# Kernel tuning notes

Hardware: AMD Instinct MI355X
Metric: run time of the kernel (lower is better)

## Reference

```python
import jax, jax.numpy as jnp
import numpy as np

D_MODEL = 1024
NUM_HEADS = 16
D_K = D_MODEL // NUM_HEADS
B, S = 4, 2048
NEG = -1e20


def setup_inputs() -> dict:
    key = jax.random.key(0)
    ks = jax.random.split(key, 12)
    def lin(kw, kb):
        # torch nn.Linear init: U(-1/sqrt(in), 1/sqrt(in)), weight shape [out, in]
        bound = 1.0 / np.sqrt(D_MODEL)
        W = jax.random.uniform(kw, (D_MODEL, D_MODEL), jnp.float32, -bound, bound)
        b = jax.random.uniform(kb, (D_MODEL,), jnp.float32, -bound, bound)
        return W, b
    Wq, bq = lin(ks[0], ks[1])
    Wk, bk = lin(ks[2], ks[3])
    Wv, bv = lin(ks[4], ks[5])
    Wo, bo = lin(ks[6], ks[7])
    q = jax.random.normal(ks[8], (B, S, D_MODEL), jnp.float32)
    k = jax.random.normal(ks[9], (B, S, D_MODEL), jnp.float32)
    v = jax.random.normal(ks[10], (B, S, D_MODEL), jnp.float32)
    # causal mask, broadcastable [1,1,S,S]; mask==0 positions are masked out
    mask = jnp.tril(jnp.ones((S, S), jnp.int32))[None, None]
    return {"q": q, "k": k, "v": v, "mask": mask,
            "Wq": Wq, "bq": bq, "Wk": Wk, "bk": bk,
            "Wv": Wv, "bv": bv, "Wo": Wo, "bo": bo}


def _split_heads(x):
    b, s, _ = x.shape
    return x.reshape(b, s, NUM_HEADS, D_K).transpose(0, 2, 1, 3)  # [b,h,s,dk]


def reference(q, k, v, mask, Wq, bq, Wk, bk, Wv, bv, Wo, bo):
    qh = _split_heads(q @ Wq.T + bq)
    kh = _split_heads(k @ Wk.T + bk)
    vh = _split_heads(v @ Wv.T + bv)
    scores = jnp.einsum('bhqd,bhkd->bhqk', qh, kh) / jnp.sqrt(jnp.float32(D_K))
    scores = jnp.where(mask == 0, jnp.float32(NEG), scores)
    attn = jax.nn.softmax(scores, axis=-1)  # dropout is identity in eval mode
    out = jnp.einsum('bhqk,bhkd->bhqd', attn, vh)
    out = out.transpose(0, 2, 1, 3).reshape(q.shape[0], -1, D_MODEL)
    return out @ Wo.T + bo, attn
```

## Files before the change

### kernel.cpp

```cpp
#include <hip/hip_runtime.h>
#include <stdint.h>

#define S_LEN 2048
#define NHEADS 16
#define DK 64
#define DMODEL 1024
#define PS_STRIDE 72
#define S_MASK -3.0e4f

typedef __bf16 bf16;
typedef __bf16 bf16x8 __attribute__((ext_vector_type(8)));
typedef float f32x4 __attribute__((ext_vector_type(4)));
typedef uint32_t u32;

#define MFMA(a, b, c) __builtin_amdgcn_mfma_f32_16x16x32_bf16((a), (b), (c), 0, 0, 0)

#define WAVE_LGKM0()                                       \
  do {                                                     \
    asm volatile("s_waitcnt lgkmcnt(0)" ::: "memory");     \
    __builtin_amdgcn_sched_barrier(0);                     \
  } while (0)
#define BAR_VM16()                                         \
  do {                                                     \
    asm volatile("s_waitcnt vmcnt(16)" ::: "memory");      \
    __builtin_amdgcn_sched_barrier(0);                     \
    __builtin_amdgcn_s_barrier();                          \
    __builtin_amdgcn_sched_barrier(0);                     \
  } while (0)

__device__ __forceinline__ bf16x8 cvt8(f32x4 a, f32x4 b) {
  bf16x8 w;
  w[0] = (bf16)a[0]; w[1] = (bf16)a[1]; w[2] = (bf16)a[2]; w[3] = (bf16)a[3];
  w[4] = (bf16)b[0]; w[5] = (bf16)b[1]; w[6] = (bf16)b[2]; w[7] = (bf16)b[3];
  return w;
}

__device__ __forceinline__ void async16(const void* g, void* lds_uniform) {
  __builtin_amdgcn_global_load_lds((const __attribute__((address_space(1))) u32*)g,
                                   (__attribute__((address_space(3))) u32*)lds_uniform,
                                   16, 0, 0);
}

__device__ __forceinline__ void stage_tile8(const bf16* gbase, size_t rstride,
                                            bf16* buf, int wave, int lane) {
  int c = wave * 64 + lane;
  int r = c >> 3, ch = c & 7;
  int chg = ch ^ (r & 7);
  const bf16* src = gbase + (size_t)r * rstride + chg * 8;
  char* dst = (char*)buf + (size_t)(wave * 64) * 16;
  async16(src, dst);
}

__global__ __launch_bounds__(256) void cvt_f32_bf16(const float* __restrict__ src,
                                                    bf16* __restrict__ dst, int n8) {
  int stride = gridDim.x * blockDim.x;
  for (int i = blockIdx.x * blockDim.x + threadIdx.x; i < n8; i += stride) {
    f32x4 a = ((const f32x4*)src)[2 * i];
    f32x4 b = ((const f32x4*)src)[2 * i + 1];
    ((bf16x8*)dst)[i] = cvt8(a, b);
  }
}

template <int MODE, typename OutT>
__global__ __launch_bounds__(256, 2) void gemm_bias(const bf16* __restrict__ X,
                                                    const bf16* __restrict__ W,
                                                    const float* __restrict__ bias,
                                                    OutT* __restrict__ out) {
  __shared__ __attribute__((aligned(16))) bf16 At[128 * 32];
  __shared__ __attribute__((aligned(16))) bf16 Bt[128 * 32];
  const int tid = threadIdx.x;
  const int wave = tid >> 6;
  const int lane = tid & 63;
  const int col16 = lane & 15;
  const int kg = lane >> 4;
  const int m0 = blockIdx.x * 128;
  const int n0 = blockIdx.y * 128;
  const int wm = (wave >> 1) * 64;
  const int wn = (wave & 1) * 64;

  f32x4 acc[4][4] = {};

  for (int k0 = 0; k0 < 1024; k0 += 32) {
    __syncthreads();
#pragma unroll
    for (int is = 0; is < 2; ++is) {
      int idx = wave * 64 + is * 256 + lane;
      int row = idx >> 2, ch = idx & 3;
      const char* ga = (const char*)(X + (size_t)(m0 + row) * 1024 + k0) + ch * 16;
      const char* gb = (const char*)(W + (size_t)(n0 + row) * 1024 + k0) + ch * 16;
      async16(ga, (char*)At + (size_t)(wave * 64 + is * 256) * 16);
      async16(gb, (char*)Bt + (size_t)(wave * 64 + is * 256) * 16);
    }
    __syncthreads();

    bf16x8 af[4], bfr[4];
#pragma unroll
    for (int i = 0; i < 4; ++i)
      af[i] = *(const bf16x8*)&At[(wm + i * 16 + col16) * 32 + kg * 8];
#pragma unroll
    for (int j = 0; j < 4; ++j)
      bfr[j] = *(const bf16x8*)&Bt[(wn + j * 16 + col16) * 32 + kg * 8];
#pragma unroll
    for (int i = 0; i < 4; ++i)
#pragma unroll
      for (int j = 0; j < 4; ++j) acc[i][j] = MFMA(af[i], bfr[j], acc[i][j]);
  }

#pragma unroll
  for (int j = 0; j < 4; ++j) {
    int n = n0 + wn + j * 16 + col16;
    float bj = bias[n];
#pragma unroll
    for (int i = 0; i < 4; ++i) {
#pragma unroll
      for (int r = 0; r < 4; ++r) {
        int m = m0 + wm + i * 16 + kg * 4 + r;
        float v = acc[i][j][r] + bj;
        size_t o;
        if (MODE == 0) {
          o = (size_t)m * 1024 + n;
        } else {
          int b = m >> 11, s = m & 2047;
          int h = n >> 6, d = n & 63;
          if (MODE == 1)
            o = ((size_t)(b * 16 + h) * 2048 + s) * 64 + d;
          else
            o = ((size_t)(b * 16 + h) * 64 + d) * 2048 + s;
        }
        out[o] = (OutT)v;
      }
    }
  }
}

__global__ __launch_bounds__(512, 4) void attn_fused(const bf16* __restrict__ Qh,
                                                     const bf16* __restrict__ Kh,
                                                     const bf16* __restrict__ Vt,
                                                     float* __restrict__ attn,
                                                     bf16* __restrict__ O) {
  __shared__ __attribute__((aligned(16))) bf16 Klds[2][64 * 64];
  __shared__ __attribute__((aligned(16))) bf16 Vlds[2][64 * 64];
  __shared__ __attribute__((aligned(16))) bf16 Ps[128 * PS_STRIDE];
  const int tid = threadIdx.x;
  const int wave = tid >> 6;
  const int lane = tid & 63;
  const int col16 = lane & 15;
  const int kg = lane >> 4;
  const int pr = blockIdx.x;
  const int bh = blockIdx.z * NHEADS + blockIdx.y;

  const bf16* qb = Qh + (size_t)bh * S_LEN * DK;
  const bf16* kb = Kh + (size_t)bh * S_LEN * DK;
  const bf16* vb = Vt + (size_t)bh * DK * S_LEN;
  float* ab = attn + (size_t)bh * S_LEN * S_LEN;
  const int b_ = bh >> 4, h_ = bh & 15;

#pragma unroll 1
  for (int sp = 0; sp < 2; ++sp) {
    const int bq = sp ? (15 - pr) : pr;
    const int q0 = bq * 128;
    const int jt_max = 2 * bq + 1;

    bf16x8 qf[2];
#pragma unroll
    for (int kk = 0; kk < 2; ++kk) {
      bf16x8 v = *(const bf16x8*)&qb[(size_t)(q0 + wave * 16 + col16) * DK + kk * 32 + kg * 8];
      bf16x8 sc;
#pragma unroll
      for (int e = 0; e < 8; ++e) sc[e] = (bf16)((float)v[e] * 0.125f);
      qf[kk] = sc;
    }

    float l_run[4] = {};

    for (int jt = 0; jt <= jt_max; ++jt) {
      const int j0 = jt * 64;
      f32x4 s[4] = {};
#pragma unroll
      for (int kk = 0; kk < 2; ++kk) {
        bf16x8 kf[4];
#pragma unroll
        for (int fc = 0; fc < 4; ++fc)
          kf[fc] = *(const bf16x8*)&kb[(size_t)(j0 + fc * 16 + col16) * DK + kk * 32 + kg * 8];
#pragma unroll
        for (int fc = 0; fc < 4; ++fc) s[fc] = MFMA(qf[kk], kf[fc], s[fc]);
      }
      if (jt >= 2 * bq) {
#pragma unroll
        for (int fc = 0; fc < 4; ++fc)
#pragma unroll
          for (int r = 0; r < 4; ++r) {
            int qi = q0 + wave * 16 + kg * 4 + r;
            int j = j0 + fc * 16 + col16;
            if (j > qi) s[fc][r] = S_MASK;
          }
      }
#pragma unroll
      for (int r = 0; r < 4; ++r)
        l_run[r] += (__expf(s[0][r]) + __expf(s[1][r])) + (__expf(s[2][r]) + __expf(s[3][r]));
    }
    float linv[4];
#pragma unroll
    for (int r = 0; r < 4; ++r) {
      float l = l_run[r];
#pragma unroll
      for (int dd = 1; dd < 16; dd <<= 1) l += __shfl_xor(l, dd, 64);
      linv[r] = 1.f / l;
    }

    {
      f32x4 z = {0.f, 0.f, 0.f, 0.f};
      for (int jt = jt_max + 1; jt < S_LEN / 64; ++jt) {
        const int j0 = jt * 64;
#pragma unroll
        for (int rep = 0; rep < 4; ++rep) {
          int idx = rep * 512 + tid;
          int row = idx >> 4, c = idx & 15;
          *(f32x4*)&ab[(size_t)(q0 + row) * S_LEN + j0 + c * 4] = z;
        }
      }
    }

    f32x4 o[4] = {};
    stage_tile8(kb, DK, Klds[0], wave, lane);
    stage_tile8(vb, S_LEN, Vlds[0], wave, lane);
    __syncthreads();
    int cur = 0;
    for (int jt = 0; jt <= jt_max; ++jt) {
      if (jt < jt_max) {
        stage_tile8(kb + (size_t)(jt + 1) * 64 * DK, DK, Klds[cur ^ 1], wave, lane);
        stage_tile8(vb + (jt + 1) * 64, S_LEN, Vlds[cur ^ 1], wave, lane);
      }
      const int j0 = jt * 64;
      f32x4 s[4] = {};
#pragma unroll
      for (int kk = 0; kk < 2; ++kk) {
        bf16x8 kf[4];
#pragma unroll
        for (int fc = 0; fc < 4; ++fc) {
          int rr = fc * 16 + col16;
          kf[fc] = *(const bf16x8*)&Klds[cur][rr * 64 + (((kk << 2) + kg) ^ (rr & 7)) * 8];
        }
#pragma unroll
        for (int fc = 0; fc < 4; ++fc) s[fc] = MFMA(qf[kk], kf[fc], s[fc]);
      }
      if (jt >= 2 * bq) {
#pragma unroll
        for (int fc = 0; fc < 4; ++fc)
#pragma unroll
          for (int r = 0; r < 4; ++r) {
            int qi = q0 + wave * 16 + kg * 4 + r;
            int j = j0 + fc * 16 + col16;
            if (j > qi) s[fc][r] = S_MASK;
          }
      }
#pragma unroll
      for (int fc = 0; fc < 4; ++fc)
#pragma unroll
        for (int r = 0; r < 4; ++r) {
          float p = __expf(s[fc][r]) * linv[r];
          int row = wave * 16 + kg * 4 + r;
          int col = fc * 16 + col16;
          ab[(size_t)(q0 + row) * S_LEN + j0 + col] = p;
          Ps[row * PS_STRIDE + col] = (bf16)p;
        }
      WAVE_LGKM0();
#pragma unroll
      for (int kk = 0; kk < 2; ++kk) {
        bf16x8 pf, vf[4];
        pf = *(const bf16x8*)&Ps[(wave * 16 + col16) * PS_STRIDE + kk * 32 + kg * 8];
#pragma unroll
        for (int fc = 0; fc < 4; ++fc) {
          int rr = fc * 16 + col16;
          vf[fc] = *(const bf16x8*)&Vlds[cur][rr * 64 + (((kk << 2) + kg) ^ (rr & 7)) * 8];
        }
#pragma unroll
        for (int fc = 0; fc < 4; ++fc) o[fc] = MFMA(pf, vf[fc], o[fc]);
      }
      BAR_VM16();
      cur ^= 1;
    }

#pragma unroll
    for (int fc = 0; fc < 4; ++fc)
#pragma unroll
      for (int r = 0; r < 4; ++r) {
        size_t row = (size_t)b_ * S_LEN + q0 + wave * 16 + kg * 4 + r;
        O[row * DMODEL + h_ * 64 + fc * 16 + col16] = (bf16)o[fc][r];
      }
    __syncthreads();
  }
}

static inline void cvt_launch(const float* src, bf16* dst, size_t n, hipStream_t stream) {
  int n8 = (int)(n / 8);
  int blocks = (n8 + 255) / 256;
  if (blocks > 2048) blocks = 2048;
  cvt_f32_bf16<<<blocks, 256, 0, stream>>>(src, dst, n8);
}

extern "C" void kernel_launch(void* const* d_in, const int* in_sizes, int n_in,
                              void* d_out, int out_size, void* d_ws, size_t ws_size,
                              hipStream_t stream) {
  (void)in_sizes; (void)n_in; (void)out_size; (void)ws_size;
  const float* q = (const float*)d_in[0];
  const float* k = (const float*)d_in[1];
  const float* v = (const float*)d_in[2];
  const float* Wq = (const float*)d_in[4];
  const float* bq = (const float*)d_in[5];
  const float* Wk = (const float*)d_in[6];
  const float* bk = (const float*)d_in[7];
  const float* Wv = (const float*)d_in[8];
  const float* bv = (const float*)d_in[9];
  const float* Wo = (const float*)d_in[10];
  const float* bo = (const float*)d_in[11];

  float* out = (float*)d_out;
  float* attn = out + (size_t)8192 * 1024;

  const size_t NX = (size_t)8192 * 1024;
  const size_t NW = (size_t)1024 * 1024;
  bf16* Qh = (bf16*)d_ws;
  bf16* Kh = Qh + NX;
  bf16* Vt = Kh + NX;
  bf16* O = Vt + NX;
  bf16* Xbf = O + NX;
  bf16* Wbf = Xbf + NX;

  dim3 gg(64, 8), bb(256);

  cvt_launch(q, Xbf, NX, stream);
  cvt_launch(Wq, Wbf, NW, stream);
  gemm_bias<1, bf16><<<gg, bb, 0, stream>>>(Xbf, Wbf, bq, Qh);

  cvt_launch(k, Xbf, NX, stream);
  cvt_launch(Wk, Wbf, NW, stream);
  gemm_bias<1, bf16><<<gg, bb, 0, stream>>>(Xbf, Wbf, bk, Kh);

  cvt_launch(v, Xbf, NX, stream);
  cvt_launch(Wv, Wbf, NW, stream);
  gemm_bias<2, bf16><<<gg, bb, 0, stream>>>(Xbf, Wbf, bv, Vt);

  attn_fused<<<dim3(8, NHEADS, 4), 512, 0, stream>>>(Qh, Kh, Vt, attn, O);

  cvt_launch(Wo, Wbf, NW, stream);
  gemm_bias<0, float><<<gg, bb, 0, stream>>>(O, Wbf, bo, out);
}
```

Baseline: 529.4 us.

## Process paired high/low query tiles jointly to share K/V tile loads

```diff
diff --git a/kernel.cpp b/kernel.cpp
--- a/kernel.cpp
+++ b/kernel.cpp
@@ -23,6 +23,13 @@
 #define BAR_VM16()                                         \
   do {                                                     \
     asm volatile("s_waitcnt vmcnt(16)" ::: "memory");      \
+    __builtin_amdgcn_sched_barrier(0);                     \
+    __builtin_amdgcn_s_barrier();                          \
+    __builtin_amdgcn_sched_barrier(0);                     \
+  } while (0)
+#define BAR_VM32()                                         \
+  do {                                                     \
+    asm volatile("s_waitcnt vmcnt(32)" ::: "memory");      \
     __builtin_amdgcn_sched_barrier(0);                     \
     __builtin_amdgcn_s_barrier();                          \
     __builtin_amdgcn_sched_barrier(0);                     \
@@ -155,141 +162,226 @@
   float* ab = attn + (size_t)bh * S_LEN * S_LEN;
   const int b_ = bh >> 4, h_ = bh & 15;
 
-#pragma unroll 1
-  for (int sp = 0; sp < 2; ++sp) {
-    const int bq = sp ? (15 - pr) : pr;
-    const int q0 = bq * 128;
-    const int jt_max = 2 * bq + 1;
-
-    bf16x8 qf[2];
-#pragma unroll
-    for (int kk = 0; kk < 2; ++kk) {
-      bf16x8 v = *(const bf16x8*)&qb[(size_t)(q0 + wave * 16 + col16) * DK + kk * 32 + kg * 8];
-      bf16x8 sc;
-#pragma unroll
-      for (int e = 0; e < 8; ++e) sc[e] = (bf16)((float)v[e] * 0.125f);
-      qf[kk] = sc;
-    }
-
-    float l_run[4] = {};
-
-    for (int jt = 0; jt <= jt_max; ++jt) {
-      const int j0 = jt * 64;
+  const int q0h = (15 - pr) * 128;
+  const int q0l = pr * 128;
+  const int jtmax_h = 31 - 2 * pr;
+  const int jtmax_l = 2 * pr + 1;
+  const int maskh0 = 30 - 2 * pr;
+  const int maskl0 = 2 * pr;
+
+  bf16x8 qfh[2], qfl[2];
+#pragma unroll
+  for (int kk = 0; kk < 2; ++kk) {
+    bf16x8 vh = *(const bf16x8*)&qb[(size_t)(q0h + wave * 16 + col16) * DK + kk * 32 + kg * 8];
+    bf16x8 vl = *(const bf16x8*)&qb[(size_t)(q0l + wave * 16 + col16) * DK + kk * 32 + kg * 8];
+    bf16x8 sh, sl;
+#pragma unroll
+    for (int e = 0; e < 8; ++e) {
+      sh[e] = (bf16)((float)vh[e] * 0.125f);
+      sl[e] = (bf16)((float)vl[e] * 0.125f);
+    }
+    qfh[kk] = sh;
+    qfl[kk] = sl;
+  }
+
+  float lh[4] = {}, ll[4] = {};
+
+  stage_tile8(kb, DK, Klds[0], wave, lane);
+  __syncthreads();
+  int cur = 0;
+  for (int jt = 0; jt <= jtmax_h; ++jt) {
+    if (jt < jtmax_h) stage_tile8(kb + (size_t)(jt + 1) * 64 * DK, DK, Klds[cur ^ 1], wave, lane);
+    const int j0 = jt * 64;
+    bf16x8 kf[2][4];
+#pragma unroll
+    for (int kk = 0; kk < 2; ++kk)
+#pragma unroll
+      for (int fc = 0; fc < 4; ++fc) {
+        int rr = fc * 16 + col16;
+        kf[kk][fc] = *(const bf16x8*)&Klds[cur][rr * 64 + (((kk << 2) + kg) ^ (rr & 7)) * 8];
+      }
+    {
       f32x4 s[4] = {};
 #pragma unroll
-      for (int kk = 0; kk < 2; ++kk) {
-        bf16x8 kf[4];
+      for (int kk = 0; kk < 2; ++kk)
+#pragma unroll
+        for (int fc = 0; fc < 4; ++fc) s[fc] = MFMA(qfh[kk], kf[kk][fc], s[fc]);
+      if (jt >= maskh0) {
 #pragma unroll
         for (int fc = 0; fc < 4; ++fc)
-          kf[fc] = *(const bf16x8*)&kb[(size_t)(j0 + fc * 16 + col16) * DK + kk * 32 + kg * 8];
-#pragma unroll
-        for (int fc = 0; fc < 4; ++fc) s[fc] = MFMA(qf[kk], kf[fc], s[fc]);
-      }
-      if (jt >= 2 * bq) {
-#pragma unroll
-        for (int fc = 0; fc < 4; ++fc)
 #pragma unroll
           for (int r = 0; r < 4; ++r) {
-            int qi = q0 + wave * 16 + kg * 4 + r;
+            int qi = q0h + wave * 16 + kg * 4 + r;
             int j = j0 + fc * 16 + col16;
             if (j > qi) s[fc][r] = S_MASK;
           }
       }
 #pragma unroll
       for (int r = 0; r < 4; ++r)
-        l_run[r] += (__expf(s[0][r]) + __expf(s[1][r])) + (__expf(s[2][r]) + __expf(s[3][r]));
-    }
-    float linv[4];
-#pragma unroll
-    for (int r = 0; r < 4; ++r) {
-      float l = l_run[r];
-#pragma unroll
-      for (int dd = 1; dd < 16; dd <<= 1) l += __shfl_xor(l, dd, 64);
-      linv[r] = 1.f / l;
-    }
-
-    {
-      f32x4 z = {0.f, 0.f, 0.f, 0.f};
-      for (int jt = jt_max + 1; jt < S_LEN / 64; ++jt) {
-        const int j0 = jt * 64;
-#pragma unroll
-        for (int rep = 0; rep < 4; ++rep) {
-          int idx = rep * 512 + tid;
-          int row = idx >> 4, c = idx & 15;
-          *(f32x4*)&ab[(size_t)(q0 + row) * S_LEN + j0 + c * 4] = z;
-        }
-      }
-    }
-
-    f32x4 o[4] = {};
-    stage_tile8(kb, DK, Klds[0], wave, lane);
-    stage_tile8(vb, S_LEN, Vlds[0], wave, lane);
-    __syncthreads();
-    int cur = 0;
-    for (int jt = 0; jt <= jt_max; ++jt) {
-      if (jt < jt_max) {
-        stage_tile8(kb + (size_t)(jt + 1) * 64 * DK, DK, Klds[cur ^ 1], wave, lane);
-        stage_tile8(vb + (jt + 1) * 64, S_LEN, Vlds[cur ^ 1], wave, lane);
-      }
-      const int j0 = jt * 64;
+        lh[r] += (__expf(s[0][r]) + __expf(s[1][r])) + (__expf(s[2][r]) + __expf(s[3][r]));
+    }
+    if (jt <= jtmax_l) {
       f32x4 s[4] = {};
 #pragma unroll
-      for (int kk = 0; kk < 2; ++kk) {
-        bf16x8 kf[4];
-#pragma unroll
-        for (int fc = 0; fc < 4; ++fc) {
-          int rr = fc * 16 + col16;
-          kf[fc] = *(const bf16x8*)&Klds[cur][rr * 64 + (((kk << 2) + kg) ^ (rr & 7)) * 8];
-        }
-#pragma unroll
-        for (int fc = 0; fc < 4; ++fc) s[fc] = MFMA(qf[kk], kf[fc], s[fc]);
-      }
-      if (jt >= 2 * bq) {
+      for (int kk = 0; kk < 2; ++kk)
+#pragma unroll
+        for (int fc = 0; fc < 4; ++fc) s[fc] = MFMA(qfl[kk], kf[kk][fc], s[fc]);
+      if (jt >= maskl0) {
 #pragma unroll
         for (int fc = 0; fc < 4; ++fc)
 #pragma unroll
           for (int r = 0; r < 4; ++r) {
-            int qi = q0 + wave * 16 + kg * 4 + r;
+            int qi = q0l + wave * 16 + kg * 4 + r;
             int j = j0 + fc * 16 + col16;
             if (j > qi) s[fc][r] = S_MASK;
           }
       }
 #pragma unroll
+      for (int r = 0; r < 4; ++r)
+        ll[r] += (__expf(s[0][r]) + __expf(s[1][r])) + (__expf(s[2][r]) + __expf(s[3][r]));
+    }
+    __syncthreads();
+    cur ^= 1;
+  }
+  float linvh[4], linvl[4];
+#pragma unroll
+  for (int r = 0; r < 4; ++r) {
+    float a = lh[r], b = ll[r];
+#pragma unroll
+    for (int dd = 1; dd < 16; dd <<= 1) {
+      a += __shfl_xor(a, dd, 64);
+      b += __shfl_xor(b, dd, 64);
+    }
+    linvh[r] = 1.f / a;
+    linvl[r] = 1.f / b;
+  }
+
+  {
+    f32x4 z = {0.f, 0.f, 0.f, 0.f};
+    for (int jt = jtmax_h + 1; jt < 32; ++jt) {
+      const int j0 = jt * 64;
+#pragma unroll
+      for (int rep = 0; rep < 4; ++rep) {
+        int idx = rep * 512 + tid;
+        int row = idx >> 4, c = idx & 15;
+        *(f32x4*)&ab[(size_t)(q0h + row) * S_LEN + j0 + c * 4] = z;
+      }
+    }
+    for (int jt = jtmax_l + 1; jt < 32; ++jt) {
+      const int j0 = jt * 64;
+#pragma unroll
+      for (int rep = 0; rep < 4; ++rep) {
+        int idx = rep * 512 + tid;
+        int row = idx >> 4, c = idx & 15;
+        *(f32x4*)&ab[(size_t)(q0l + row) * S_LEN + j0 + c * 4] = z;
+      }
+    }
+  }
+
+  f32x4 oh[4] = {}, ol[4] = {};
+  stage_tile8(kb, DK, Klds[0], wave, lane);
+  stage_tile8(vb, S_LEN, Vlds[0], wave, lane);
+  __syncthreads();
+  cur = 0;
+  for (int jt = 0; jt <= jtmax_h; ++jt) {
+    if (jt < jtmax_h) {
+      stage_tile8(kb + (size_t)(jt + 1) * 64 * DK, DK, Klds[cur ^ 1], wave, lane);
+      stage_tile8(vb + (jt + 1) * 64, S_LEN, Vlds[cur ^ 1], wave, lane);
+    }
+    const int j0 = jt * 64;
+    bf16x8 kf[2][4], vf[2][4];
+#pragma unroll
+    for (int kk = 0; kk < 2; ++kk)
+#pragma unroll
+      for (int fc = 0; fc < 4; ++fc) {
+        int rr = fc * 16 + col16;
+        int sw = (((kk << 2) + kg) ^ (rr & 7)) * 8;
+        kf[kk][fc] = *(const bf16x8*)&Klds[cur][rr * 64 + sw];
+        vf[kk][fc] = *(const bf16x8*)&Vlds[cur][rr * 64 + sw];
+      }
+    {
+      f32x4 s[4] = {};
+#pragma unroll
+      for (int kk = 0; kk < 2; ++kk)
+#pragma unroll
+        for (int fc = 0; fc < 4; ++fc) s[fc] = MFMA(qfh[kk], kf[kk][fc], s[fc]);
+      if (jt >= maskh0) {
+#pragma unroll
+        for (int fc = 0; fc < 4; ++fc)
+#pragma unroll
+          for (int r = 0; r < 4; ++r) {
+            int qi = q0h + wave * 16 + kg * 4 + r;
+            int j = j0 + fc * 16 + col16;
+            if (j > qi) s[fc][r] = S_MASK;
+          }
+      }
+#pragma unroll
       for (int fc = 0; fc < 4; ++fc)
 #pragma unroll
         for (int r = 0; r < 4; ++r) {
-          float p = __expf(s[fc][r]) * linv[r];
+          float p = __expf(s[fc][r]) * linvh[r];
           int row = wave * 16 + kg * 4 + r;
           int col = fc * 16 + col16;
-          ab[(size_t)(q0 + row) * S_LEN + j0 + col] = p;
+          ab[(size_t)(q0h + row) * S_LEN + j0 + col] = p;
           Ps[row * PS_STRIDE + col] = (bf16)p;
         }
       WAVE_LGKM0();
 #pragma unroll
       for (int kk = 0; kk < 2; ++kk) {
-        bf16x8 pf, vf[4];
-        pf = *(const bf16x8*)&Ps[(wave * 16 + col16) * PS_STRIDE + kk * 32 + kg * 8];
-#pragma unroll
-        for (int fc = 0; fc < 4; ++fc) {
-          int rr = fc * 16 + col16;
-          vf[fc] = *(const bf16x8*)&Vlds[cur][rr * 64 + (((kk << 2) + kg) ^ (rr & 7)) * 8];
+        bf16x8 pf = *(const bf16x8*)&Ps[(wave * 16 + col16) * PS_STRIDE + kk * 32 + kg * 8];
+#pragma unroll
+        for (int fc = 0; fc < 4; ++fc) oh[fc] = MFMA(pf, vf[kk][fc], oh[fc]);
+      }
+    }
+    if (jt <= jtmax_l) {
+      f32x4 s[4] = {};
+#pragma unroll
+      for (int kk = 0; kk < 2; ++kk)
+#pragma unroll
+        for (int fc = 0; fc < 4; ++fc) s[fc] = MFMA(qfl[kk], kf[kk][fc], s[fc]);
+      if (jt >= maskl0) {
+#pragma unroll
+        for (int fc = 0; fc < 4; ++fc)
+#pragma unroll
+          for (int r = 0; r < 4; ++r) {
+            int qi = q0l + wave * 16 + kg * 4 + r;
+            int j = j0 + fc * 16 + col16;
+            if (j > qi) s[fc][r] = S_MASK;
+          }
+      }
+#pragma unroll
+      for (int fc = 0; fc < 4; ++fc)
+#pragma unroll
+        for (int r = 0; r < 4; ++r) {
+          float p = __expf(s[fc][r]) * linvl[r];
+          int row = wave * 16 + kg * 4 + r;
+          int col = fc * 16 + col16;
+          ab[(size_t)(q0l + row) * S_LEN + j0 + col] = p;
+          Ps[row * PS_STRIDE + col] = (bf16)p;
         }
-#pragma unroll
-        for (int fc = 0; fc < 4; ++fc) o[fc] = MFMA(pf, vf[fc], o[fc]);
-      }
+      WAVE_LGKM0();
+#pragma unroll
+      for (int kk = 0; kk < 2; ++kk) {
+        bf16x8 pf = *(const bf16x8*)&Ps[(wave * 16 + col16) * PS_STRIDE + kk * 32 + kg * 8];
+#pragma unroll
+        for (int fc = 0; fc < 4; ++fc) ol[fc] = MFMA(pf, vf[kk][fc], ol[fc]);
+      }
+      BAR_VM32();
+    } else {
       BAR_VM16();
-      cur ^= 1;
-    }
-
-#pragma unroll
-    for (int fc = 0; fc < 4; ++fc)
-#pragma unroll
-      for (int r = 0; r < 4; ++r) {
-        size_t row = (size_t)b_ * S_LEN + q0 + wave * 16 + kg * 4 + r;
-        O[row * DMODEL + h_ * 64 + fc * 16 + col16] = (bf16)o[fc][r];
-      }
-    __syncthreads();
-  }
+    }
+    cur ^= 1;
+  }
+
+#pragma unroll
+  for (int fc = 0; fc < 4; ++fc)
+#pragma unroll
+    for (int r = 0; r < 4; ++r) {
+      size_t rowh = (size_t)b_ * S_LEN + q0h + wave * 16 + kg * 4 + r;
+      size_t rowl = (size_t)b_ * S_LEN + q0l + wave * 16 + kg * 4 + r;
+      O[rowh * DMODEL + h_ * 64 + fc * 16 + col16] = (bf16)oh[fc][r];
+      O[rowl * DMODEL + h_ * 64 + fc * 16 + col16] = (bf16)ol[fc][r];
+    }
 }
 
 static inline void cvt_launch(const float* src, bf16* dst, size_t n, hipStream_t stream) {
```

New measurement: 664.3 us. +25.5%, slower.
